# Kernel optimization log

Measured on AMD Instinct MI355X. Metric: run time of the kernel, lower is better.

## Reference

```python
import jax, jax.numpy as jnp
import numpy as np

N_NODES = 100000
N_EDGES = 4000000
CHANNELS = 64


def setup_inputs() -> dict:
    key = jax.random.key(0)
    k1, k2, k3, k4, k5 = jax.random.split(key, 5)
    x = jax.random.normal(k1, (N_NODES, CHANNELS), dtype=jnp.float32)
    sources = jax.random.randint(k2, (N_EDGES,), 0, N_NODES, dtype=jnp.int64)
    targets = jax.random.randint(k3, (N_EDGES,), 0, N_NODES, dtype=jnp.int64)
    norm = jax.random.uniform(k4, (N_NODES, 1), dtype=jnp.float32)
    # xavier_normal_ for a (64, 64) weight: std = sqrt(2 / (fan_in + fan_out))
    std = float(np.sqrt(2.0 / (CHANNELS + CHANNELS)))
    weight = jax.random.normal(k5, (CHANNELS, CHANNELS), dtype=jnp.float32) * std
    return {"x": x, "sources": sources, "targets": targets, "norm": norm, "weight": weight}


def reference(x, sources, targets, norm, weight):
    # x.index_add(0, targets, x[sources]) == x + segment_sum(x[sources], targets)
    messages = x[sources]  # [E, C] gather
    agg = x + jax.ops.segment_sum(messages, targets, num_segments=x.shape[0])  # [N, C]
    h = norm * agg  # per-node scale, norm broadcasts [N,1] over [N,C]
    return h @ weight  # [N, C]
```

## Files before the change

### kernel.cpp

```cpp
#include <hip/hip_runtime.h>


constexpr int C = 64;
constexpr int BN = 128;
constexpr int CHUNK2 = 8192;
constexpr int MAXB = 1024;
constexpr int NPASS = 7;
constexpr int BINS = BN * 8;
constexpr int ASTRIDE = 65;
constexpr int UNI = BN * ASTRIDE;
constexpr int TAILCAP = 65536;

__global__ __launch_bounds__(256) void init_kernel(
    int* __restrict__ cursor, int* __restrict__ tailcnt, int NB, int slot) {
  int i = blockIdx.x * 256 + threadIdx.x;
  if (i < NB) cursor[i] = i * slot;
  if (i == NB) *tailcnt = 0;
}

__global__ __launch_bounds__(512) void binfused_kernel(
    const int* __restrict__ src, const int* __restrict__ tgt,
    int* __restrict__ gcursor, int* __restrict__ tailcnt,
    unsigned* __restrict__ tailrec, unsigned* __restrict__ recs,
    const float* __restrict__ x, unsigned* __restrict__ xb,
    int E, int NB, int slot, int binBlocks, int total8) {
  if ((int)blockIdx.x >= binBlocks) {
    int i = (blockIdx.x - binBlocks) * 512 + threadIdx.x;
    if (i < total8) {
      const float4* x4 = (const float4*)x;
      float4 a = x4[i * 2], bq = x4[i * 2 + 1];
      float f[8] = {a.x, a.y, a.z, a.w, bq.x, bq.y, bq.z, bq.w};
      unsigned w[4];
#pragma unroll
      for (int k = 0; k < 4; k++) {
        unsigned u0 = __float_as_uint(f[2 * k]);
        unsigned u1 = __float_as_uint(f[2 * k + 1]);
        u0 = (u0 + 0x7FFFu + ((u0 >> 16) & 1u)) >> 16;
        u1 = (u1 + 0x7FFFu + ((u1 >> 16) & 1u)) >> 16;
        w[k] = u0 | (u1 << 16);
      }
      ((uint4*)xb)[i] = make_uint4(w[0], w[1], w[2], w[3]);
    }
    return;
  }
  __shared__ unsigned rec[CHUNK2];
  __shared__ unsigned bi[CHUNK2];
  __shared__ int hist[MAXB];
  __shared__ int gb[MAXB];
  int tid = threadIdx.x;
  int base = blockIdx.x * CHUNK2;
  int count = E - base; if (count > CHUNK2) count = CHUNK2;

  for (int i = tid; i < NB; i += 512) hist[i] = 0;
  __syncthreads();
  int nv = count >> 2;
  const int4* s4 = (const int4*)(src + base);
  const int4* t4 = (const int4*)(tgt + base);
  for (int i = tid; i < nv; i += 512) {
    int4 s = s4[i], t = t4[i];
    unsigned r0 = ((unsigned)s.x << 7) | (unsigned)(t.x & 127);
    unsigned r1 = ((unsigned)s.y << 7) | (unsigned)(t.y & 127);
    unsigned r2 = ((unsigned)s.z << 7) | (unsigned)(t.z & 127);
    unsigned r3 = ((unsigned)s.w << 7) | (unsigned)(t.w & 127);
    ((uint4*)rec)[i] = make_uint4(r0, r1, r2, r3);
    int b0 = t.x >> 7, b1 = t.y >> 7, b2 = t.z >> 7, b3 = t.w >> 7;
    unsigned i0 = (unsigned)atomicAdd(&hist[b0], 1);
    unsigned i1 = (unsigned)atomicAdd(&hist[b1], 1);
    unsigned i2 = (unsigned)atomicAdd(&hist[b2], 1);
    unsigned i3 = (unsigned)atomicAdd(&hist[b3], 1);
    ((uint4*)bi)[i] = make_uint4(((unsigned)b0 << 13) | i0,
                                 ((unsigned)b1 << 13) | i1,
                                 ((unsigned)b2 << 13) | i2,
                                 ((unsigned)b3 << 13) | i3);
  }
  for (int i = (nv << 2) + tid; i < count; i += 512) {
    int s = src[base + i], t = tgt[base + i];
    int b = t >> 7;
    rec[i] = ((unsigned)s << 7) | (unsigned)(t & 127);
    unsigned ix = (unsigned)atomicAdd(&hist[b], 1);
    bi[i] = ((unsigned)b << 13) | ix;
  }
  __syncthreads();
  for (int i = tid; i < NB; i += 512) {
    int c = hist[i];
    gb[i] = c ? atomicAdd(&gcursor[i], c) : 0;
  }
  __syncthreads();
  for (int i = tid; i < count; i += 512) {
    unsigned v = bi[i];
    int b = (int)(v >> 13);
    int dest = gb[b] + (int)(v & 8191u);
    if (dest < (b + 1) * slot) {
      recs[dest] = rec[i];
    } else {
      int tp = atomicAdd(tailcnt, 1);
      if (tp < TAILCAP) {
        tailrec[2 * tp] = rec[i];
        tailrec[2 * tp + 1] = (unsigned)b;
      }
    }
  }
}

__device__ __forceinline__ void acc8_bf16(float (&a)[8], uint4 v) {
  a[0] += __uint_as_float(v.x << 16);
  a[1] += __uint_as_float(v.x & 0xFFFF0000u);
  a[2] += __uint_as_float(v.y << 16);
  a[3] += __uint_as_float(v.y & 0xFFFF0000u);
  a[4] += __uint_as_float(v.z << 16);
  a[5] += __uint_as_float(v.z & 0xFFFF0000u);
  a[6] += __uint_as_float(v.w << 16);
  a[7] += __uint_as_float(v.w & 0xFFFF0000u);
}

__device__ __forceinline__ void acc8_f32(float (&a)[8], float4 u, float4 v) {
  a[0] += u.x; a[1] += u.y; a[2] += u.z; a[3] += u.w;
  a[4] += v.x; a[5] += v.y; a[6] += v.z; a[7] += v.w;
}

template <bool USE_BF16>
__global__ __launch_bounds__(512) void sortgather_kernel(
    const float* __restrict__ x, const unsigned* __restrict__ xb,
    const unsigned* __restrict__ recs, const int* __restrict__ cursor,
    const int* __restrict__ tailcnt, const unsigned* __restrict__ tailrec,
    const float* __restrict__ norm, const float* __restrict__ W,
    float* __restrict__ out, int N, int slot) {
  __shared__ int cnt[BINS];
  __shared__ int pre[512];
  __shared__ int nst[BINS + 1];
  __shared__ float uni[UNI];
  unsigned* sorted = (unsigned*)uni;
  float* accum = uni;
  int tid = threadIdx.x;
  int lane = tid & 63;
  int wave = tid >> 6;
  int b = blockIdx.x;
  int n0 = b * BN;
  int nn = N - n0; if (nn > BN) nn = BN;
  int beg = b * slot;
  int m = cursor[b] - beg; if (m > slot) m = slot;
  int end = beg + m;

  unsigned myrec[16];
#pragma unroll
  for (int j = 0; j < 16; j++) {
    int r = beg + tid + j * 512;
    myrec[j] = (r < end) ? recs[r] : 0xFFFFFFFFu;
  }
  cnt[tid] = 0; cnt[tid + 512] = 0;
  __syncthreads();
#pragma unroll
  for (int j = 0; j < 16; j++) {
    unsigned rc = myrec[j];
    if (rc != 0xFFFFFFFFu) {
      int q = (int)(rc >> 21); if (q > 6) q = 6;
      atomicAdd(&cnt[((int)(rc & 127u) << 3) | q], 1);
    }
  }
  __syncthreads();
  int c0 = cnt[2 * tid], c1 = cnt[2 * tid + 1];
  pre[tid] = c0 + c1;
  __syncthreads();
  for (int off = 1; off < 512; off <<= 1) {
    int v = pre[tid];
    int a = (tid >= off) ? pre[tid - off] : 0;
    __syncthreads();
    pre[tid] = v + a;
    __syncthreads();
  }
  {
    int run = pre[tid] - (c0 + c1);
    nst[2 * tid] = run;
    nst[2 * tid + 1] = run + c0;
    cnt[2 * tid] = run;
    cnt[2 * tid + 1] = run + c0;
  }
  if (tid == 0) nst[BINS] = m;
  __syncthreads();
#pragma unroll
  for (int j = 0; j < 16; j++) {
    unsigned rc = myrec[j];
    if (rc != 0xFFFFFFFFu) {
      int q = (int)(rc >> 21); if (q > 6) q = 6;
      int p = atomicAdd(&cnt[((int)(rc & 127u) << 3) | q], 1);
      sorted[p] = rc >> 7;
    }
  }
  __syncthreads();

  int l7 = tid & 7;
  int g  = tid >> 3;
  int k0 = g, k1 = g + 64;
  bool has0 = k0 < nn, has1 = k1 < nn;
  const float4* x4 = (const float4*)x;
  const uint4* xb4 = (const uint4*)xb;

  float a0[8], a1[8];
  if (has0) {
    float4 u = x4[(n0 + k0) * 16 + l7 * 2], v = x4[(n0 + k0) * 16 + l7 * 2 + 1];
    a0[0] = u.x; a0[1] = u.y; a0[2] = u.z; a0[3] = u.w;
    a0[4] = v.x; a0[5] = v.y; a0[6] = v.z; a0[7] = v.w;
  } else {
#pragma unroll
    for (int j = 0; j < 8; j++) a0[j] = 0.0f;
  }
  if (has1) {
    float4 u = x4[(n0 + k1) * 16 + l7 * 2], v = x4[(n0 + k1) * 16 + l7 * 2 + 1];
    a1[0] = u.x; a1[1] = u.y; a1[2] = u.z; a1[3] = u.w;
    a1[4] = v.x; a1[5] = v.y; a1[6] = v.z; a1[7] = v.w;
  } else {
#pragma unroll
    for (int j = 0; j < 8; j++) a1[j] = 0.0f;
  }

  for (int p = 0; p < NPASS; p++) {
    if (has0) {
      int e = nst[k0 * 8 + p], ge = nst[k0 * 8 + p + 1];
      for (; e + 1 < ge; e += 2) {
        int s0 = (int)sorted[e], s1 = (int)sorted[e + 1];
        if (USE_BF16) {
          uint4 v0 = xb4[s0 * 8 + l7];
          uint4 v1 = xb4[s1 * 8 + l7];
          acc8_bf16(a0, v0); acc8_bf16(a0, v1);
        } else {
          float4 u0 = x4[s0 * 16 + l7 * 2], w0 = x4[s0 * 16 + l7 * 2 + 1];
          float4 u1 = x4[s1 * 16 + l7 * 2], w1 = x4[s1 * 16 + l7 * 2 + 1];
          acc8_f32(a0, u0, w0); acc8_f32(a0, u1, w1);
        }
      }
      if (e < ge) {
        int s = (int)sorted[e];
        if (USE_BF16) { uint4 v = xb4[s * 8 + l7]; acc8_bf16(a0, v); }
        else { acc8_f32(a0, x4[s * 16 + l7 * 2], x4[s * 16 + l7 * 2 + 1]); }
      }
    }
    if (has1) {
      int e = nst[k1 * 8 + p], ge = nst[k1 * 8 + p + 1];
      for (; e + 1 < ge; e += 2) {
        int s0 = (int)sorted[e], s1 = (int)sorted[e + 1];
        if (USE_BF16) {
          uint4 v0 = xb4[s0 * 8 + l7];
          uint4 v1 = xb4[s1 * 8 + l7];
          acc8_bf16(a1, v0); acc8_bf16(a1, v1);
        } else {
          float4 u0 = x4[s0 * 16 + l7 * 2], w0 = x4[s0 * 16 + l7 * 2 + 1];
          float4 u1 = x4[s1 * 16 + l7 * 2], w1 = x4[s1 * 16 + l7 * 2 + 1];
          acc8_f32(a1, u0, w0); acc8_f32(a1, u1, w1);
        }
      }
      if (e < ge) {
        int s = (int)sorted[e];
        if (USE_BF16) { uint4 v = xb4[s * 8 + l7]; acc8_bf16(a1, v); }
        else { acc8_f32(a1, x4[s * 16 + l7 * 2], x4[s * 16 + l7 * 2 + 1]); }
      }
    }
  }

  {
    int tc = *tailcnt; if (tc > TAILCAP) tc = TAILCAP;
    for (int r = 0; r < tc; r++) {
      if ((int)tailrec[2 * r + 1] != b) continue;
      unsigned rc = tailrec[2 * r];
      int tl = (int)(rc & 127u);
      if (tl == k0 || tl == k1) {
        int s = (int)(rc >> 7);
        if (USE_BF16) {
          uint4 v = xb4[s * 8 + l7];
          if (tl == k0) acc8_bf16(a0, v); else acc8_bf16(a1, v);
        } else {
          float4 u = x4[s * 16 + l7 * 2], w = x4[s * 16 + l7 * 2 + 1];
          if (tl == k0) acc8_f32(a0, u, w); else acc8_f32(a1, u, w);
        }
      }
    }
  }
  __syncthreads();

  if (has0) {
#pragma unroll
    for (int j = 0; j < 8; j++) accum[k0 * ASTRIDE + 8 * l7 + j] = a0[j];
  }
  if (has1) {
#pragma unroll
    for (int j = 0; j < 8; j++) accum[k1 * ASTRIDE + 8 * l7 + j] = a1[j];
  }
  __syncthreads();

  float wreg[C];
#pragma unroll
  for (int k = 0; k < C; k++) wreg[k] = W[k * C + lane];

  for (int i = wave; i < nn; i += 8) {
    int n = n0 + i;
    float a = accum[i * ASTRIDE + lane];
    float o = 0.0f;
#pragma unroll
    for (int c = 0; c < C; c++)
      o = fmaf(__shfl(a, c, 64), wreg[c], o);
    out[n * C + lane] = o * norm[n];
  }
}

extern "C" void kernel_launch(void* const* d_in, const int* in_sizes, int n_in,
                              void* d_out, int out_size, void* d_ws, size_t ws_size,
                              hipStream_t stream) {
  const float* x       = (const float*)d_in[0];
  const int*   sources = (const int*)d_in[1];
  const int*   targets = (const int*)d_in[2];
  const float* norm    = (const float*)d_in[3];
  const float* weight  = (const float*)d_in[4];
  float* out = (float*)d_out;

  int N = in_sizes[0] / C;
  int E = in_sizes[1];
  int NB = (N + BN - 1) / BN;

  size_t availw = ws_size / 4;
  size_t xw = (size_t)N * C / 2;
  size_t fixedw = (size_t)NB + 1 + 2 * (size_t)TAILCAP;
  bool use_bf16; int slot;
  if (availw >= xw + fixedw + (size_t)NB * 8192) { use_bf16 = true; slot = 8192; }
  else if (availw >= xw + fixedw + (size_t)NB * 6144) { use_bf16 = true; slot = 6144; }
  else {
    use_bf16 = false;
    size_t s = (availw > fixedw) ? (availw - fixedw) / (size_t)NB : 0;
    slot = s > 8192 ? 8192 : (int)s;
  }

  unsigned* xb; int* cursor;
  if (use_bf16) {
    xb = (unsigned*)d_ws;
    cursor = (int*)d_ws + xw;
  } else {
    xb = nullptr;
    cursor = (int*)d_ws;
  }
  int* tailcnt = cursor + NB;
  unsigned* tailrec = (unsigned*)(tailcnt + 1);
  unsigned* recs = tailrec + 2 * (size_t)TAILCAP;

  int hb = (E + CHUNK2 - 1) / CHUNK2;
  int total8 = N * C / 8;
  int cvtBlocks = use_bf16 ? (total8 + 511) / 512 : 0;

  init_kernel<<<(NB + 256) / 256, 256, 0, stream>>>(cursor, tailcnt, NB, slot);
  binfused_kernel<<<hb + cvtBlocks, 512, 0, stream>>>(
      sources, targets, cursor, tailcnt, tailrec, recs, x, xb,
      E, NB, slot, hb, total8);
  if (use_bf16) {
    sortgather_kernel<true><<<NB, 512, 0, stream>>>(
        x, xb, recs, cursor, tailcnt, tailrec, norm, weight, out, N, slot);
  } else {
    sortgather_kernel<false><<<NB, 512, 0, stream>>>(
        x, xb, recs, cursor, tailcnt, tailrec, norm, weight, out, N, slot);
  }
}
```

Baseline: 287.3 us.

## Locally sort binned edges in shared memory and pad global bin cursors

The binning kernel now keeps edge records in registers, computes a block-wide prefix scan over bin histograms, and scatters records into shared memory sorted by bin. The final write-out then walks that bin-sorted order, so consecutive threads write contiguous runs of each bin's global slot and stores coalesce better. Global per-bin cursors are padded to a stride of 32 ints so atomics from different blocks on neighbouring bins no longer hit the same cache line. In exchange the kernel adds a 512-step scan with many syncs and uses more workspace for the padded cursor array.

After: 284.0 us. Within noise of the previous version (-1.2%).

```diff
diff --git a/kernel.cpp b/kernel.cpp
--- a/kernel.cpp
+++ b/kernel.cpp
@@ -10,11 +10,12 @@
 constexpr int ASTRIDE = 65;
 constexpr int UNI = BN * ASTRIDE;
 constexpr int TAILCAP = 65536;
+constexpr int CSTR = 32;
 
 __global__ __launch_bounds__(256) void init_kernel(
     int* __restrict__ cursor, int* __restrict__ tailcnt, int NB, int slot) {
   int i = blockIdx.x * 256 + threadIdx.x;
-  if (i < NB) cursor[i] = i * slot;
+  if (i < NB) cursor[i * CSTR] = i * slot;
   if (i == NB) *tailcnt = 0;
 }
 
@@ -43,59 +44,101 @@
     }
     return;
   }
-  __shared__ unsigned rec[CHUNK2];
-  __shared__ unsigned bi[CHUNK2];
+  __shared__ unsigned rs[CHUNK2];
+  __shared__ unsigned short sb[CHUNK2];
   __shared__ int hist[MAXB];
   __shared__ int gb[MAXB];
+  __shared__ int cbase[MAXB];
+  __shared__ int pre[512];
   int tid = threadIdx.x;
   int base = blockIdx.x * CHUNK2;
   int count = E - base; if (count > CHUNK2) count = CHUNK2;
 
-  for (int i = tid; i < NB; i += 512) hist[i] = 0;
-  __syncthreads();
+  for (int i = tid; i < MAXB; i += 512) hist[i] = 0;
+  __syncthreads();
+
+  unsigned mrec[16];
+  unsigned mbix[16];
   int nv = count >> 2;
+  int rem = count & 3;
   const int4* s4 = (const int4*)(src + base);
   const int4* t4 = (const int4*)(tgt + base);
-  for (int i = tid; i < nv; i += 512) {
-    int4 s = s4[i], t = t4[i];
-    unsigned r0 = ((unsigned)s.x << 7) | (unsigned)(t.x & 127);
-    unsigned r1 = ((unsigned)s.y << 7) | (unsigned)(t.y & 127);
-    unsigned r2 = ((unsigned)s.z << 7) | (unsigned)(t.z & 127);
-    unsigned r3 = ((unsigned)s.w << 7) | (unsigned)(t.w & 127);
-    ((uint4*)rec)[i] = make_uint4(r0, r1, r2, r3);
-    int b0 = t.x >> 7, b1 = t.y >> 7, b2 = t.z >> 7, b3 = t.w >> 7;
-    unsigned i0 = (unsigned)atomicAdd(&hist[b0], 1);
-    unsigned i1 = (unsigned)atomicAdd(&hist[b1], 1);
-    unsigned i2 = (unsigned)atomicAdd(&hist[b2], 1);
-    unsigned i3 = (unsigned)atomicAdd(&hist[b3], 1);
-    ((uint4*)bi)[i] = make_uint4(((unsigned)b0 << 13) | i0,
-                                 ((unsigned)b1 << 13) | i1,
-                                 ((unsigned)b2 << 13) | i2,
-                                 ((unsigned)b3 << 13) | i3);
-  }
-  for (int i = (nv << 2) + tid; i < count; i += 512) {
+#pragma unroll
+  for (int j = 0; j < 4; j++) {
+    int i = tid + j * 512;
+    if (i < nv) {
+      int4 s = s4[i], t = t4[i];
+      int b0 = t.x >> 7, b1 = t.y >> 7, b2 = t.z >> 7, b3 = t.w >> 7;
+      mrec[4 * j + 0] = ((unsigned)s.x << 7) | (unsigned)(t.x & 127);
+      mrec[4 * j + 1] = ((unsigned)s.y << 7) | (unsigned)(t.y & 127);
+      mrec[4 * j + 2] = ((unsigned)s.z << 7) | (unsigned)(t.z & 127);
+      mrec[4 * j + 3] = ((unsigned)s.w << 7) | (unsigned)(t.w & 127);
+      mbix[4 * j + 0] = ((unsigned)b0 << 13) | (unsigned)atomicAdd(&hist[b0], 1);
+      mbix[4 * j + 1] = ((unsigned)b1 << 13) | (unsigned)atomicAdd(&hist[b1], 1);
+      mbix[4 * j + 2] = ((unsigned)b2 << 13) | (unsigned)atomicAdd(&hist[b2], 1);
+      mbix[4 * j + 3] = ((unsigned)b3 << 13) | (unsigned)atomicAdd(&hist[b3], 1);
+    } else {
+#pragma unroll
+      for (int k = 0; k < 4; k++) mbix[4 * j + k] = 0xFFFFFFFFu;
+    }
+  }
+  unsigned trec = 0, tbix = 0xFFFFFFFFu;
+  if (tid < rem) {
+    int i = (nv << 2) + tid;
     int s = src[base + i], t = tgt[base + i];
     int b = t >> 7;
-    rec[i] = ((unsigned)s << 7) | (unsigned)(t & 127);
-    unsigned ix = (unsigned)atomicAdd(&hist[b], 1);
-    bi[i] = ((unsigned)b << 13) | ix;
-  }
-  __syncthreads();
-  for (int i = tid; i < NB; i += 512) {
-    int c = hist[i];
-    gb[i] = c ? atomicAdd(&gcursor[i], c) : 0;
-  }
-  __syncthreads();
+    trec = ((unsigned)s << 7) | (unsigned)(t & 127);
+    tbix = ((unsigned)b << 13) | (unsigned)atomicAdd(&hist[b], 1);
+  }
+  __syncthreads();
+
+  int c0 = hist[2 * tid], c1 = hist[2 * tid + 1];
+  pre[tid] = c0 + c1;
+  __syncthreads();
+  for (int off = 1; off < 512; off <<= 1) {
+    int v = pre[tid];
+    int a = (tid >= off) ? pre[tid - off] : 0;
+    __syncthreads();
+    pre[tid] = v + a;
+    __syncthreads();
+  }
+  {
+    int run = pre[tid] - (c0 + c1);
+    cbase[2 * tid] = run;
+    cbase[2 * tid + 1] = run + c0;
+  }
+  if (2 * tid < NB && c0) gb[2 * tid] = atomicAdd(&gcursor[2 * tid * CSTR], c0);
+  if (2 * tid + 1 < NB && c1)
+    gb[2 * tid + 1] = atomicAdd(&gcursor[(2 * tid + 1) * CSTR], c1);
+  __syncthreads();
+
+#pragma unroll
+  for (int j = 0; j < 16; j++) {
+    unsigned v = mbix[j];
+    if (v != 0xFFFFFFFFu) {
+      int b = (int)(v >> 13);
+      int pos = cbase[b] + (int)(v & 8191u);
+      rs[pos] = mrec[j];
+      sb[pos] = (unsigned short)b;
+    }
+  }
+  if (tbix != 0xFFFFFFFFu) {
+    int b = (int)(tbix >> 13);
+    int pos = cbase[b] + (int)(tbix & 8191u);
+    rs[pos] = trec;
+    sb[pos] = (unsigned short)b;
+  }
+  __syncthreads();
+
   for (int i = tid; i < count; i += 512) {
-    unsigned v = bi[i];
-    int b = (int)(v >> 13);
-    int dest = gb[b] + (int)(v & 8191u);
+    int b = (int)sb[i];
+    int dest = gb[b] + (i - cbase[b]);
     if (dest < (b + 1) * slot) {
-      recs[dest] = rec[i];
+      recs[dest] = rs[i];
     } else {
       int tp = atomicAdd(tailcnt, 1);
       if (tp < TAILCAP) {
-        tailrec[2 * tp] = rec[i];
+        tailrec[2 * tp] = rs[i];
         tailrec[2 * tp + 1] = (unsigned)b;
       }
     }
@@ -138,7 +181,7 @@
   int n0 = b * BN;
   int nn = N - n0; if (nn > BN) nn = BN;
   int beg = b * slot;
-  int m = cursor[b] - beg; if (m > slot) m = slot;
+  int m = cursor[b * CSTR] - beg; if (m > slot) m = slot;
   int end = beg + m;
 
   unsigned myrec[16];
@@ -317,7 +360,7 @@
 
   size_t availw = ws_size / 4;
   size_t xw = (size_t)N * C / 2;
-  size_t fixedw = (size_t)NB + 1 + 2 * (size_t)TAILCAP;
+  size_t fixedw = (size_t)NB * CSTR + 1 + 2 * (size_t)TAILCAP;
   bool use_bf16; int slot;
   if (availw >= xw + fixedw + (size_t)NB * 8192) { use_bf16 = true; slot = 8192; }
   else if (availw >= xw + fixedw + (size_t)NB * 6144) { use_bf16 = true; slot = 6144; }
@@ -335,7 +378,7 @@
     xb = nullptr;
     cursor = (int*)d_ws;
   }
-  int* tailcnt = cursor + NB;
+  int* tailcnt = cursor + (size_t)NB * CSTR;
   unsigned* tailrec = (unsigned*)(tailcnt + 1);
   unsigned* recs = tailrec + 2 * (size_t)TAILCAP;
 
```
